# Kernel tuning notes

Measured on AMD Instinct MI355X. Metric: run time of the kernel, lower is better.

Reference implementation:

```python
import jax, jax.numpy as jnp
import numpy as np
jax.config.update("jax_enable_x64", True)  # int64 hash codes for lattice keys

N_KPTS = 32768
C = 61      # feature channels; f-MLP input dim is C+3 = 64
D = 64      # disp-distribution channels
D_LAT = 8   # last f-layer output -> permutohedral position dim

# large odd 62-bit multipliers for the lattice-key hash (wraps mod 2^64)
_MULTS = np.array([2654435761405764093, 1181783497276652981,
                   3202034522624059733, 2685821657736338717,
                   1876998521354586173, 1481765933965188213,
                   2549297995355413921, 3373259426345127233], dtype=np.int64)


def _hcode(k, mults):
    return jnp.sum(k.astype(jnp.int64) * mults, axis=-1)


def _pl_filter(pos, vals):
    """Permutohedral lattice splat -> blur -> slice (approx. Gaussian filter).
    pos: (N, d) float32 lattice positions, vals: (N, vd) float32 values."""
    N, d = pos.shape
    vd = vals.shape[1]
    M = N * (d + 1)  # fixed-size hash table (every point touches d+1 vertices)
    # --- elevate onto hyperplane H_d in R^{d+1} ---
    scale = np.float32(np.sqrt(2.0 / 3.0) * (d + 1)) / np.sqrt(
        np.arange(1, d + 1, dtype=np.float32) * np.arange(2, d + 2, dtype=np.float32))
    E = np.zeros((d + 1, d), dtype=np.float32)
    E[0, :] = 1.0
    for i in range(1, d + 1):
        E[i, i - 1] = -float(i)
        E[i, i:] = 1.0
    elevated = (pos * jnp.asarray(scale, jnp.float32)) @ jnp.asarray(E).T  # (N, d+1)
    # --- nearest zero-colored lattice point and simplex ranks ---
    rem0 = jnp.floor(elevated / (d + 1) + 0.5) * (d + 1)
    sum_val = jnp.round(jnp.sum(rem0, -1) / (d + 1)).astype(jnp.int32)
    diff = elevated - rem0
    rank = jnp.argsort(jnp.argsort(-diff, axis=-1), axis=-1).astype(jnp.int32) + sum_val[:, None]
    lo = rank < 0
    hi = rank > d
    rem0 = rem0 + jnp.where(lo, float(d + 1), 0.0) - jnp.where(hi, float(d + 1), 0.0)
    rank = rank + jnp.where(lo, d + 1, 0) - jnp.where(hi, d + 1, 0)
    # --- barycentric coordinates ---
    t = (elevated - rem0) / (d + 1)
    rows = jnp.arange(N)[:, None]
    bary = jnp.zeros((N, d + 2), jnp.float32)
    bary = bary.at[rows, d - rank].add(t)
    bary = bary.at[rows, d + 1 - rank].add(-t)
    bary = bary.at[:, 0].add(1.0 + bary[:, d + 1])
    w = bary[:, :d + 1]  # (N, d+1) vertex weights
    # --- simplex vertex keys (first d coords; full key sums to 0) ---
    canonical = np.zeros((d + 1, d + 1), np.int32)
    for r in range(d + 1):
        canonical[r, :d + 1 - r] = r
        canonical[r, d + 1 - r:] = r - (d + 1)
    keys = rem0.astype(jnp.int32)[None, :, :d] + jnp.asarray(canonical)[:, rank[:, :d]]  # (d+1,N,d)
    # --- hash table via sorted unique codes (jit-safe fixed size) ---
    mults = jnp.asarray(_MULTS[:d])
    codes = _hcode(keys, mults).reshape(M)
    uniq, inv = jnp.unique(codes, return_inverse=True, size=M,
                           fill_value=jnp.iinfo(jnp.int64).max)
    inv = inv.reshape(M)
    # --- splat ---
    wv = (w.T[:, :, None] * vals[None]).reshape(M, vd)
    lat = jax.ops.segment_sum(wv, inv, num_segments=M)  # (M, vd)
    occ = jax.ops.segment_sum(jnp.ones((M,), jnp.float32), inv, num_segments=M) > 0
    ukeys = jnp.zeros((M, d), jnp.int32).at[inv].set(keys.reshape(M, d))
    # --- blur along each of the d+1 lattice directions ---
    for j in range(d + 1):
        off = np.ones(d + 1, np.int32)
        off[j] = -d
        o = jnp.asarray(off[:d])
        def _nbr(sign, lat=lat):
            c = _hcode(ukeys + sign * o, mults)
            i = jnp.clip(jnp.searchsorted(uniq, c), 0, M - 1)
            ok = (jnp.take(uniq, i) == c) & jnp.take(occ, i)
            return jnp.where(ok[:, None], jnp.take(lat, i, axis=0), 0.0)
        lat = jnp.where(occ[:, None], 0.5 * lat + 0.25 * (_nbr(1) + _nbr(-1)), lat)
    # --- slice ---
    alpha = 1.0 / (1.0 + 2.0 ** (-d))
    return jnp.sum(w.T[:, :, None] * jnp.take(lat, inv, axis=0).reshape(d + 1, N, vd), 0) * alpha


def _layernorm2(x, g, b):
    # LayerNorm(normalized_shape=(N, K)): stats over the last TWO dims jointly
    mu = jnp.mean(x, axis=(-2, -1), keepdims=True)
    var = jnp.mean((x - mu) ** 2, axis=(-2, -1), keepdims=True)
    return (x - mu) * jax.lax.rsqrt(var + 1e-5) * g + b


def setup_inputs() -> dict:
    key = jax.random.key(0)
    ks = jax.random.split(key, 16)
    f32 = jnp.float32
    rn = lambda k, shape, s=1.0: jax.random.normal(k, shape, dtype=f32) * s
    inp = {
        "kpts": rn(ks[0], (1, N_KPTS, 3)),
        "disps_distr": rn(ks[1], (1, N_KPTS, D)),
        "feats": rn(ks[2], (1, N_KPTS, C)),
    }
    i = 3
    for b in range(2):
        inp[f"Wd{b}0"] = rn(ks[i], (D, D), 0.05); i += 1
        inp[f"bd{b}0"] = jnp.zeros((D,), f32)
        inp[f"Wd{b}1"] = rn(ks[i], (D, D), 0.05); i += 1
        inp[f"bd{b}1"] = jnp.zeros((D,), f32)
        inp[f"Wf{b}"] = rn(ks[i], (C + 3, D_LAT), 0.1); i += 1
        inp[f"bf{b}"] = jnp.zeros((D_LAT,), f32)
        inp[f"g{b}"] = jnp.ones((N_KPTS, D_LAT), f32)
        inp[f"be{b}"] = jnp.zeros((N_KPTS, D_LAT), f32)
    return inp


def reference(kpts, disps_distr, feats, Wd00, bd00, Wd01, bd01, Wf0, bf0, g0, be0,
              Wd10, bd10, Wd11, bd11, Wf1, bf1, g1, be1):
    fk = jnp.concatenate([kpts, feats], axis=-1)  # (1, N, C+3)
    x = jnp.reshape(disps_distr, (1, N_KPTS, -1))
    blocks = [(Wd00, bd00, Wd01, bd01, Wf0, bf0, g0, be0),
              (Wd10, bd10, Wd11, bd11, Wf1, bf1, g1, be1)]
    for (Wd0, bd0, Wd1, bd1, Wf, bf, g, be) in blocks:
        x = jax.nn.relu(x @ Wd0 + bd0)   # d-layer 0
        x = jax.nn.relu(x @ Wd1 + bd1)   # d-layer 1
        # only the LAST f-layer output is used by the torch code (feats_kpts is never updated)
        pos = _layernorm2(jax.nn.relu(fk @ Wf + bf), g, be)  # (1, N, 8)
        x = _pl_filter(pos[0], x[0])[None]
    return x
```

## Files before the change

kernel.cpp:

```cpp
#include <hip/hip_runtime.h>
#include <hip/hip_bf16.h>
#include <hip/hip_fp16.h>
#include <stdint.h>

typedef unsigned long long u64;

#define NK 32768
#define DL 8
#define DP1 9
#define MT (NK*DP1)
#define HBITS 19
#define HSIZE (1u<<HBITS)
#define HMASK (HSIZE-1)
#define EMPTY_CODE 0xFFFFFFFFFFFFFFFFULL
#define NBLK 1152
#define HBLK (HSIZE/256)
#define CAP 32
#define MAXHUB 16384

__device__ __constant__ u64 c_mults[8] = {
    2654435761405764093ULL, 1181783497276652981ULL, 3202034522624059733ULL,
    2685821657736338717ULL, 1876998521354586173ULL, 1481765933965188213ULL,
    2549297995355413921ULL, 3373259426345127233ULL};

__device__ __forceinline__ unsigned int hmix(u64 x) {
    return (unsigned int)(x >> (64 - HBITS)) & HMASK;
}

__device__ __forceinline__ u64 dir_delta(int j) {
    u64 s = 0;
    #pragma unroll
    for (int k = 0; k < 8; k++) s += c_mults[k];
    return (j == 8) ? s : (s - 9ULL * c_mults[j]);
}

__device__ __forceinline__ float ldf(const void* p, int i, int bf) {
    if (bf) return __bfloat162float(((const __hip_bfloat16*)p)[i]);
    return ((const float*)p)[i];
}

__global__ void k_detect(const unsigned* __restrict__ g0w, int* __restrict__ flag) {
    if (threadIdx.x == 0) {
        int f = 1;
        for (int i = 0; i < 8; i++) if (g0w[i] != 0x3F803F80u) f = 0;
        *flag = f;
    }
}

__global__ __launch_bounds__(256) void k_mlp(const void* __restrict__ xin, int use_df_in,
    const void* __restrict__ W0, const void* __restrict__ B0,
    const void* __restrict__ W1, const void* __restrict__ B1,
    float* __restrict__ xout, const int* __restrict__ df, double* __restrict__ stats) {
    __shared__ float w0[64*64], w1[64*64], xs[16][64], y1[16][64];
    int bf = *df;
    int bfin = use_df_in ? bf : 0;
    int tid = threadIdx.x;
    int row0 = blockIdx.x * 16;
    if (blockIdx.x == 0 && tid == 0) { stats[0] = 0.0; stats[1] = 0.0; }
    for (int i = tid; i < 4096; i += 256) { w0[i] = ldf(W0, i, bf); w1[i] = ldf(W1, i, bf); }
    for (int i = tid; i < 1024; i += 256) xs[i>>6][i&63] = ldf(xin, row0*64 + i, bfin);
    __syncthreads();
    int rb = tid >> 6, col = tid & 63;
    float b0c = ldf(B0, col, bf);
    float a0 = b0c, a1 = b0c, a2 = b0c, a3 = b0c;
    #pragma unroll
    for (int k = 0; k < 64; k++) {
        float w = w0[k*64+col];
        a0 = fmaf(xs[rb   ][k], w, a0);
        a1 = fmaf(xs[rb+ 4][k], w, a1);
        a2 = fmaf(xs[rb+ 8][k], w, a2);
        a3 = fmaf(xs[rb+12][k], w, a3);
    }
    y1[rb   ][col] = fmaxf(a0, 0.f);
    y1[rb+ 4][col] = fmaxf(a1, 0.f);
    y1[rb+ 8][col] = fmaxf(a2, 0.f);
    y1[rb+12][col] = fmaxf(a3, 0.f);
    __syncthreads();
    float b1c = ldf(B1, col, bf);
    a0 = b1c; a1 = b1c; a2 = b1c; a3 = b1c;
    #pragma unroll
    for (int k = 0; k < 64; k++) {
        float w = w1[k*64+col];
        a0 = fmaf(y1[rb   ][k], w, a0);
        a1 = fmaf(y1[rb+ 4][k], w, a1);
        a2 = fmaf(y1[rb+ 8][k], w, a2);
        a3 = fmaf(y1[rb+12][k], w, a3);
    }
    xout[(row0+rb   )*64 + col] = fmaxf(a0, 0.f);
    xout[(row0+rb+ 4)*64 + col] = fmaxf(a1, 0.f);
    xout[(row0+rb+ 8)*64 + col] = fmaxf(a2, 0.f);
    xout[(row0+rb+12)*64 + col] = fmaxf(a3, 0.f);
}

__global__ __launch_bounds__(256) void k_pos(const void* __restrict__ kpts,
    const void* __restrict__ feats, const void* __restrict__ Wf,
    const void* __restrict__ Bf, float* __restrict__ pos_pre,
    double* __restrict__ stats, const int* __restrict__ df) {
    __shared__ float wf[64*8];
    __shared__ float fk[32][65];
    __shared__ float red[256], red2[256];
    int bf = *df;
    int tid = threadIdx.x;
    int n0 = blockIdx.x * 32;
    for (int i = tid; i < 512; i += 256) wf[i] = ldf(Wf, i, bf);
    for (int i = tid; i < 32*64; i += 256) {
        int pt = i >> 6, k = i & 63, n = n0 + pt;
        fk[pt][k] = (k < 3) ? ldf(kpts, n*3 + k, bf) : ldf(feats, n*61 + (k-3), bf);
    }
    __syncthreads();
    int pt = tid >> 3, j = tid & 7, n = n0 + pt;
    float acc = ldf(Bf, j, bf);
    #pragma unroll
    for (int k = 0; k < 64; k++) acc = fmaf(fk[pt][k], wf[k*8+j], acc);
    acc = fmaxf(acc, 0.f);
    pos_pre[n*8 + j] = acc;
    red[tid] = acc; red2[tid] = acc * acc;
    __syncthreads();
    for (int s = 128; s > 0; s >>= 1) {
        if (tid < s) { red[tid] += red[tid+s]; red2[tid] += red2[tid+s]; }
        __syncthreads();
    }
    if (tid == 0) { atomicAdd(&stats[0], (double)red[0]); atomicAdd(&stats[1], (double)red2[0]); }
}

__global__ __launch_bounds__(256) void k_embed(const float* __restrict__ pos_pre,
    const double* __restrict__ stats, const void* __restrict__ g,
    const void* __restrict__ be, float* __restrict__ wgt,
    u64* __restrict__ pcodes, int* __restrict__ cnt, int* __restrict__ cnt2,
    int* __restrict__ hubid, const int* __restrict__ df) {
    int bf = *df;
    int n = blockIdx.x * 256 + threadIdx.x;
    if (n >= NK) return;
    const double inv_cnt = 1.0 / (double)(NK * DL);
    double mud = stats[0] * inv_cnt;
    double vard = stats[1] * inv_cnt - mud * mud;
    float mu = (float)mud;
    float rs = rsqrtf((float)vard + 1e-5f);
    const float scale[8] = {
        5.196152422706632f, 3.0f, 2.1213203435596424f, 1.643167672515498f,
        1.3416407864998738f, 1.1338934190276817f, 0.9819805060619657f, 0.8660254037844386f};
    float c[8];
    #pragma unroll
    for (int k = 0; k < 8; k++) {
        float v = pos_pre[n*8 + k];
        float p = (v - mu) * rs * ldf(g, n*8 + k, bf) + ldf(be, n*8 + k, bf);
        c[k] = p * scale[k];
    }
    float sufa[9]; sufa[8] = 0.f;
    #pragma unroll
    for (int k = 7; k >= 0; k--) sufa[k] = sufa[k+1] + c[k];
    float elev[9];
    elev[0] = sufa[0];
    #pragma unroll
    for (int i = 1; i < 9; i++) elev[i] = sufa[i] - (float)i * c[i-1];
    int ri[9], sumv = 0;
    float diff[9];
    #pragma unroll
    for (int i = 0; i < 9; i++) {
        ri[i] = (int)floorf(elev[i] / 9.0f + 0.5f);
        sumv += ri[i];
        diff[i] = elev[i] - 9.f * (float)ri[i];
    }
    int rank[9];
    #pragma unroll
    for (int i = 0; i < 9; i++) {
        int r = 0;
        #pragma unroll
        for (int j = 0; j < 9; j++)
            r += (diff[j] > diff[i]) || ((diff[j] == diff[i]) && (j < i));
        rank[i] = r + sumv;
    }
    #pragma unroll
    for (int i = 0; i < 9; i++) {
        if (rank[i] < 0)      { rank[i] += 9; ri[i] += 1; }
        else if (rank[i] > 8) { rank[i] -= 9; ri[i] -= 1; }
    }
    float t[9];
    #pragma unroll
    for (int i = 0; i < 9; i++) t[i] = (elev[i] - 9.f * (float)ri[i]) / 9.f;
    float bary[10];
    #pragma unroll
    for (int i = 0; i < 10; i++) bary[i] = 0.f;
    #pragma unroll
    for (int i = 0; i < 9; i++) { bary[8 - rank[i]] += t[i]; bary[9 - rank[i]] -= t[i]; }
    bary[0] += 1.f + bary[9];
    for (int r = 0; r < 9; r++) {
        u64 code = 0;
        #pragma unroll
        for (int k = 0; k < 8; k++) {
            int key = 9 * ri[k] + ((rank[k] <= 8 - r) ? r : (r - 9));
            code += (u64)(long long)key * c_mults[k];
        }
        int m = n * 9 + r;
        wgt[m] = bary[r];
        pcodes[m] = code;
        cnt[m] = 0;
        cnt2[m] = 0;
        hubid[m] = -1;
    }
}

__global__ __launch_bounds__(256) void k_insert(const u64* __restrict__ pcodes,
    u64* __restrict__ htab_code, unsigned int* __restrict__ ppos) {
    int m = blockIdx.x * 256 + threadIdx.x;
    if (m >= MT) return;
    u64 code = pcodes[m];
    unsigned int pos = hmix(code);
    for (;;) {
        u64 cc = htab_code[pos];
        if (cc == code) break;
        if (cc == EMPTY_CODE) {
            u64 old = atomicCAS(&htab_code[pos], EMPTY_CODE, code);
            if (old == EMPTY_CODE || old == code) break;
        }
        pos = (pos + 1) & HMASK;
    }
    ppos[m] = pos;
}

__global__ __launch_bounds__(256) void k_occ(const u64* __restrict__ htab_code,
    int* __restrict__ bocc) {
    __shared__ int wcnt[4];
    unsigned int i = blockIdx.x * 256 + threadIdx.x;
    bool occ = (htab_code[i] != EMPTY_CODE);
    u64 mask = __ballot(occ);
    int lane = threadIdx.x & 63;
    if (lane == 0) wcnt[threadIdx.x >> 6] = __popcll(mask);
    __syncthreads();
    if (threadIdx.x == 0) bocc[blockIdx.x] = wcnt[0] + wcnt[1] + wcnt[2] + wcnt[3];
}

__global__ __launch_bounds__(256) void k_occscan(int* __restrict__ bocc,
    int* __restrict__ counter, int* __restrict__ nhub) {
    __shared__ int s[256];
    __shared__ int carry;
    int t = threadIdx.x;
    if (t == 0) { carry = 0; *nhub = 0; }
    __syncthreads();
    for (int c = 0; c < HBLK / 256; c++) {
        int i = c * 256 + t;
        int v = bocc[i];
        s[t] = v; __syncthreads();
        for (int off = 1; off < 256; off <<= 1) {
            int a = (t >= off) ? s[t-off] : 0;
            __syncthreads();
            s[t] += a;
            __syncthreads();
        }
        int cl = carry;
        bocc[i] = s[t] - v + cl;
        __syncthreads();
        if (t == 0) carry = cl + s[255];
        __syncthreads();
    }
    if (t == 0) *counter = carry;
}

__global__ __launch_bounds__(256) void k_assign2(const u64* __restrict__ htab_code,
    const int* __restrict__ bocc, int* __restrict__ htab_slot,
    u64* __restrict__ slot_code) {
    __shared__ int wbase[4];
    unsigned int i = blockIdx.x * 256 + threadIdx.x;
    u64 cde = htab_code[i];
    bool occ = (cde != EMPTY_CODE);
    int lane = threadIdx.x & 63;
    int wid  = threadIdx.x >> 6;
    u64 mask = __ballot(occ);
    int prefix = __popcll(mask & ((1ULL << lane) - 1ULL));
    if (lane == 0) wbase[wid] = __popcll(mask);
    __syncthreads();
    if (threadIdx.x == 0) {
        int run = bocc[blockIdx.x];
        for (int w = 0; w < 4; w++) { int c = wbase[w]; wbase[w] = run; run += c; }
    }
    __syncthreads();
    if (occ) {
        int s = wbase[wid] + prefix;
        htab_slot[i] = s;
        slot_code[s] = cde;
    }
}

__global__ __launch_bounds__(256) void k_nbr(const u64* __restrict__ slot_code,
    const u64* __restrict__ htab_code, const int* __restrict__ htab_slot,
    const int* __restrict__ counter, int2* __restrict__ nbr) {
    int idx = blockIdx.x * 256 + threadIdx.x;
    if (idx >= 9 * MT) return;
    int j = idx / MT;
    int sl = idx - j * MT;
    int count = *counter;
    if (sl >= count) return;
    u64 dj = dir_delta(j);
    u64 code = slot_code[sl];
    int res[2];
    #pragma unroll
    for (int s = 0; s < 2; s++) {
        u64 cde = code + (s ? (u64)(0ULL - dj) : dj);
        unsigned int pos = hmix(cde);
        int r = -1;
        for (;;) {
            u64 cc = htab_code[pos];
            if (cc == cde) { r = htab_slot[pos]; break; }
            if (cc == EMPTY_CODE) break;
            pos = (pos + 1) & HMASK;
        }
        res[s] = r;
    }
    nbr[j * MT + sl] = make_int2(res[0], res[1]);
}

__global__ __launch_bounds__(256) void k_lookup(const unsigned int* __restrict__ ppos,
    const int* __restrict__ htab_slot, int* __restrict__ sidx, int* __restrict__ cnt) {
    int m = blockIdx.x * 256 + threadIdx.x;
    if (m >= MT) return;
    int s = htab_slot[ppos[m]];
    sidx[m] = s;
    atomicAdd(&cnt[s], 1);
}

__global__ __launch_bounds__(256) void k_scan1(const int* __restrict__ cnt,
    int* __restrict__ exbuf, int* __restrict__ bsum,
    int* __restrict__ hublist, int* __restrict__ hubid, int* __restrict__ nhub) {
    __shared__ int s[256];
    int t = threadIdx.x;
    int i = blockIdx.x * 256 + t;
    int v = cnt[i];
    if (v > CAP) {
        int h = atomicAdd(nhub, 1);
        if (h < MAXHUB) { hublist[h] = i; hubid[i] = h; }
    }
    s[t] = v; __syncthreads();
    for (int off = 1; off < 256; off <<= 1) {
        int a = (t >= off) ? s[t-off] : 0;
        __syncthreads();
        s[t] += a;
        __syncthreads();
    }
    exbuf[i] = s[t] - v;
    if (t == 255) bsum[blockIdx.x] = s[255];
}

__global__ __launch_bounds__(256) void k_scan2(int* __restrict__ bsum) {
    __shared__ int s[256];
    __shared__ int carry;
    int t = threadIdx.x;
    if (t == 0) carry = 0;
    __syncthreads();
    for (int c = 0; c < (NBLK + 255) / 256; c++) {
        int i = c * 256 + t;
        int v = (i < NBLK) ? bsum[i] : 0;
        s[t] = v; __syncthreads();
        for (int off = 1; off < 256; off <<= 1) {
            int a = (t >= off) ? s[t-off] : 0;
            __syncthreads();
            s[t] += a;
            __syncthreads();
        }
        int cl = carry;
        if (i < NBLK) bsum[i] = s[t] - v + cl;
        __syncthreads();
        if (t == 0) carry = cl + s[255];
        __syncthreads();
    }
}

__global__ __launch_bounds__(256) void k_scatter(const int* __restrict__ sidx,
    const int* __restrict__ exbuf, const int* __restrict__ bsum,
    int* __restrict__ cnt2, int* __restrict__ list) {
    int m = blockIdx.x * 256 + threadIdx.x;
    if (m < MT) {
        int s = sidx[m];
        int ofs = atomicAdd(&cnt2[s], 1);
        list[exbuf[s] + bsum[s >> 8] + ofs] = m;
    }
}

__global__ __launch_bounds__(256) void k_splat_a(const float* __restrict__ xbuf,
    const float* __restrict__ wgt, const int* __restrict__ exbuf,
    const int* __restrict__ bsum, const int* __restrict__ cnt,
    const int* __restrict__ list, __half* __restrict__ val,
    const int* __restrict__ counter) {
    int count = *counter;
    int sl = blockIdx.x * 8 + (threadIdx.x >> 5);
    int lane = threadIdx.x & 31;
    if (sl >= count) return;
    int c = cnt[sl];
    if (c > CAP) return;
    int st = exbuf[sl] + bsum[sl >> 8];
    const float2* x2 = (const float2*)xbuf;
    float2 acc = make_float2(0.f, 0.f);
    int mm = 0; float ww = 0.f;
    if (lane < c) { mm = list[st + lane]; ww = wgt[mm]; }
    for (int k = 0; k < c; k++) {
        int   m = __shfl(mm, k, 32);
        float w = __shfl(ww, k, 32);
        float2 xv = x2[(m / 9) * 32 + lane];
        acc.x = fmaf(w, xv.x, acc.x);
        acc.y = fmaf(w, xv.y, acc.y);
    }
    ((__half2*)val)[(size_t)sl * 32 + lane] = __float22half2_rn(acc);
}

__global__ __launch_bounds__(256) void k_splat_b(const float* __restrict__ xbuf,
    const float* __restrict__ wgt, const int* __restrict__ sidx,
    const int* __restrict__ cnt, const int* __restrict__ list,
    const int* __restrict__ hubid, float* __restrict__ hubval) {
    int chunk = blockIdx.x * 8 + (threadIdx.x >> 5);
    int lane = threadIdx.x & 31;
    int e = chunk * 32 + lane;
    int m = 0, hid = -1; float w = 0.f; int hub = 0;
    if (e < MT) {
        m = list[e];
        int slot = sidx[m];
        hub = (cnt[slot] > CAP);
        if (hub) { w = wgt[m]; hid = hubid[slot]; }
    }
    u64 bal = __ballot(hub);
    unsigned int half = (threadIdx.x & 32) ? (unsigned int)(bal >> 32) : (unsigned int)bal;
    if (!half) return;
    const float2* x2 = (const float2*)xbuf;
    float2 acc = make_float2(0.f, 0.f);
    int cur = -1;
    while (half) {
        int k = __ffs(half) - 1; half &= half - 1;
        int   hk = __shfl(hid, k, 32);
        int   mk = __shfl(m, k, 32);
        float wk = __shfl(w, k, 32);
        float2 xv = x2[(mk / 9) * 32 + lane];
        if (hk != cur) {
            if (cur >= 0) {
                atomicAdd(&hubval[(size_t)cur * 64 + 2*lane    ], acc.x);
                atomicAdd(&hubval[(size_t)cur * 64 + 2*lane + 1], acc.y);
            }
            cur = hk; acc = make_float2(0.f, 0.f);
        }
        acc.x = fmaf(wk, xv.x, acc.x);
        acc.y = fmaf(wk, xv.y, acc.y);
    }
    atomicAdd(&hubval[(size_t)cur * 64 + 2*lane    ], acc.x);
    atomicAdd(&hubval[(size_t)cur * 64 + 2*lane + 1], acc.y);
}

__global__ __launch_bounds__(256) void k_hubcvt(const float* __restrict__ hubval,
    const int* __restrict__ hublist, const int* __restrict__ nhub,
    __half* __restrict__ val) {
    int idx = blockIdx.x * 256 + threadIdx.x;
    int hi = idx >> 5, lane = idx & 31;
    if (hi >= *nhub) return;
    int sl = hublist[hi];
    float2 v = ((const float2*)hubval)[(size_t)hi * 32 + lane];
    ((__half2*)val)[(size_t)sl * 32 + lane] = __float22half2_rn(v);
}

__global__ __launch_bounds__(256) void k_blur(const __half* __restrict__ vin,
    __half* __restrict__ vout, const int2* __restrict__ nbrj,
    const int* __restrict__ counter) {
    int idx = blockIdx.x * 256 + threadIdx.x;
    int sl = idx >> 3, lane = idx & 7;
    int count = *counter;
    if (sl >= count) return;
    int2 nbp = nbrj[sl];
    typedef union { uint4 u; __half2 h[4]; } row16;
    const uint4* vin4 = (const uint4*)vin;
    uint4* vout4 = (uint4*)vout;
    row16 S, A, B, O;
    S.u = vin4[(size_t)sl*8 + lane];
    uint4 z; z.x = 0; z.y = 0; z.z = 0; z.w = 0;
    A.u = (nbp.x >= 0) ? vin4[(size_t)nbp.x*8 + lane] : z;
    B.u = (nbp.y >= 0) ? vin4[(size_t)nbp.y*8 + lane] : z;
    #pragma unroll
    for (int k = 0; k < 4; k++) {
        float2 fs = __half22float2(S.h[k]);
        float2 fa = __half22float2(A.h[k]);
        float2 fb = __half22float2(B.h[k]);
        float2 r;
        r.x = 0.5f * fs.x + 0.25f * (fa.x + fb.x);
        r.y = 0.5f * fs.y + 0.25f * (fa.y + fb.y);
        O.h[k] = __float22half2_rn(r);
    }
    vout4[(size_t)sl*8 + lane] = O.u;
}

__global__ __launch_bounds__(256) void k_slice(const float* __restrict__ wgt,
    const int* __restrict__ sidx, const __half* __restrict__ val,
    float* __restrict__ outf, void* __restrict__ outb, int write_out,
    const int* __restrict__ df) {
    int bf = *df;
    int idx = blockIdx.x * 256 + threadIdx.x;
    if (idx >= NK * 64) return;
    int n = idx >> 6, ch = idx & 63;
    float acc = 0.f;
    #pragma unroll
    for (int r = 0; r < 9; r++) {
        int m = n * 9 + r;
        acc = fmaf(wgt[m], __half2float(val[(size_t)sidx[m]*64 + ch]), acc);
    }
    acc *= 0.9961089494163424f;
    if (write_out) {
        if (bf) ((__hip_bfloat16*)outb)[idx] = __float2bfloat16(acc);
        else    ((float*)outb)[idx] = acc;
    } else {
        outf[idx] = acc;
    }
}

extern "C" void kernel_launch(void* const* d_in, const int* in_sizes, int n_in,
                              void* d_out, int out_size, void* d_ws, size_t ws_size,
                              hipStream_t stream) {
    const void* kpts  = d_in[0];
    const void* disps = d_in[1];
    const void* feats = d_in[2];

    char* p = (char*)d_ws;
    float* xbuf     = (float*)p;  p += (size_t)NK*64*4;
    float* pos_pre  = (float*)p;  p += (size_t)NK*8*4;
    double* stats   = (double*)p; p += 256;
    int*   dflag    = (int*)p;    p += 256;
    float* wgt      = (float*)p;  p += (size_t)MT*4;
    int*   sidx     = (int*)p;    p += (size_t)MT*4;
    u64*   pcodes   = (u64*)p;    p += (size_t)MT*8;
    unsigned int* ppos = (unsigned int*)p; p += (size_t)MT*4;
    u64*   htabc    = (u64*)p;    p += (size_t)HSIZE*8;
    int*   htabs    = (int*)p;    p += (size_t)HSIZE*4;
    u64*   slotc    = (u64*)p;    p += (size_t)MT*8;
    int*   counter  = (int*)p;    p += 256;
    int*   nhub     = (int*)p;    p += 256;
    int*   bocc     = (int*)p;    p += (size_t)HBLK*4;
    int*   cnt      = (int*)p;    p += (size_t)MT*4;
    int*   cnt2     = (int*)p;    p += (size_t)MT*4;
    int*   hubid    = (int*)p;    p += (size_t)MT*4;
    int*   exbuf    = (int*)p;    p += (size_t)MT*4;
    int*   list     = (int*)p;    p += (size_t)MT*4;
    int*   bsum     = (int*)p;    p += 256*32;
    int*   hublist  = (int*)p;    p += (size_t)MAXHUB*4;
    float* hubval   = (float*)p;  p += (size_t)MAXHUB*64*4;
    int2*  nbr      = (int2*)p;   p += (size_t)MT*9*8;
    __half* valA    = (__half*)p; p += (size_t)MT*64*2;
    __half* valB    = (__half*)p; p += (size_t)MT*64*2;

    k_detect<<<1, 64, 0, stream>>>((const unsigned*)d_in[3 + 6], dflag);

    for (int b = 0; b < 2; b++) {
        const void* W0 = d_in[3 + b*8 + 0];
        const void* B0 = d_in[3 + b*8 + 1];
        const void* W1 = d_in[3 + b*8 + 2];
        const void* B1 = d_in[3 + b*8 + 3];
        const void* Wf = d_in[3 + b*8 + 4];
        const void* Bf = d_in[3 + b*8 + 5];
        const void* G  = d_in[3 + b*8 + 6];
        const void* Be = d_in[3 + b*8 + 7];

        k_mlp<<<NK/16, 256, 0, stream>>>(b == 0 ? disps : (const void*)xbuf, b == 0 ? 1 : 0,
                                         W0, B0, W1, B1, xbuf, dflag, stats);

        k_pos<<<NK/32, 256, 0, stream>>>(kpts, feats, Wf, Bf, pos_pre, stats, dflag);

        hipMemsetAsync(htabc, 0xFF, (size_t)HSIZE*8, stream);
        hipMemsetAsync(hubval, 0, (size_t)MAXHUB*64*4, stream);

        k_embed<<<NK/256, 256, 0, stream>>>(pos_pre, stats, G, Be, wgt, pcodes,
                                            cnt, cnt2, hubid, dflag);
        k_insert<<<NBLK, 256, 0, stream>>>(pcodes, htabc, ppos);
        k_occ<<<HBLK, 256, 0, stream>>>(htabc, bocc);
        k_occscan<<<1, 256, 0, stream>>>(bocc, counter, nhub);
        k_assign2<<<HBLK, 256, 0, stream>>>(htabc, bocc, htabs, slotc);
        k_nbr<<<(9*MT + 255)/256, 256, 0, stream>>>(slotc, htabc, htabs, counter, nbr);
        k_lookup<<<NBLK, 256, 0, stream>>>(ppos, htabs, sidx, cnt);

        k_scan1<<<NBLK, 256, 0, stream>>>(cnt, exbuf, bsum, hublist, hubid, nhub);
        k_scan2<<<1, 256, 0, stream>>>(bsum);
        k_scatter<<<NBLK, 256, 0, stream>>>(sidx, exbuf, bsum, cnt2, list);
        k_splat_a<<<(MT + 7)/8, 256, 0, stream>>>(xbuf, wgt, exbuf, bsum, cnt, list,
                                                  valA, counter);
        k_splat_b<<<(MT/32 + 7)/8, 256, 0, stream>>>(xbuf, wgt, sidx, cnt, list, hubid, hubval);
        k_hubcvt<<<(MAXHUB*32)/256, 256, 0, stream>>>(hubval, hublist, nhub, valA);

        for (int j = 0; j < 9; j++) {
            const __half* vin = (j & 1) ? valB : valA;
            __half*       vout = (j & 1) ? valA : valB;
            k_blur<<<(MT*8 + 255)/256, 256, 0, stream>>>(vin, vout, nbr + (size_t)j*MT, counter);
        }
        k_slice<<<(NK*64)/256, 256, 0, stream>>>(wgt, sidx, valB, xbuf,
                                                 d_out, b == 1 ? 1 : 0, dflag);
    }
}
```

Before: 774.6 us.

## Merge independent kernels and run blur chain in persistent grid-barrier kernel

Independent kernels (MLP+pos, embed+memsets, nbr+lookup, splat_a+splat_b) are merged into single launches that branch on block index. The hub conversion, the nine blur passes and the slice are fused into one persistent kernel with a software grid barrier, cutting per-block launch overhead and gaps. The persistent kernel uses 1024 blocks and relies on all of them being co-resident; without a cooperative launch this could deadlock if occupancy is lower than assumed. Stats reset moves into the coop kernel for the next block iteration.

```diff
diff --git a/kernel.cpp b/kernel.cpp
--- a/kernel.cpp
+++ b/kernel.cpp
@@ -18,6 +18,16 @@
 #define CAP 32
 #define MAXHUB 16384
 
+#define MLPB (NK/16)
+#define POSB (NK/32)
+#define EMBB (NK/256)
+#define HZB  384
+#define VZB  128
+#define NBRB (9*MT/256)
+#define SPAB (MT/8)
+#define SPBB 1152
+#define COOPB 1024
+
 __device__ __constant__ u64 c_mults[8] = {
     2654435761405764093ULL, 1181783497276652981ULL, 3202034522624059733ULL,
     2685821657736338717ULL, 1876998521354586173ULL, 1481765933965188213ULL,
@@ -39,97 +49,132 @@
     return ((const float*)p)[i];
 }
 
-__global__ void k_detect(const unsigned* __restrict__ g0w, int* __restrict__ flag) {
+__device__ __forceinline__ void gbar(int* bar, int* s_gen) {
+    __syncthreads();
+    if (threadIdx.x == 0) {
+        int g = *s_gen;
+        int nb = (int)gridDim.x;
+        __builtin_amdgcn_fence(__ATOMIC_RELEASE, "agent");
+        int v = __hip_atomic_fetch_add(&bar[0], 1, __ATOMIC_ACQ_REL, __HIP_MEMORY_SCOPE_AGENT);
+        if (v == nb - 1) {
+            __hip_atomic_fetch_add(&bar[0], -nb, __ATOMIC_RELAXED, __HIP_MEMORY_SCOPE_AGENT);
+            __hip_atomic_store(&bar[1], g + 1, __ATOMIC_RELEASE, __HIP_MEMORY_SCOPE_AGENT);
+        } else {
+            while (__hip_atomic_load(&bar[1], __ATOMIC_RELAXED, __HIP_MEMORY_SCOPE_AGENT) == g) {
+                __builtin_amdgcn_s_sleep(8);
+            }
+        }
+        __builtin_amdgcn_fence(__ATOMIC_ACQUIRE, "agent");
+        *s_gen = g + 1;
+    }
+    __syncthreads();
+}
+
+__global__ void k_detect(const unsigned* __restrict__ g0w, int* __restrict__ flag,
+                         double* __restrict__ stats, int* __restrict__ bar) {
     if (threadIdx.x == 0) {
         int f = 1;
         for (int i = 0; i < 8; i++) if (g0w[i] != 0x3F803F80u) f = 0;
         *flag = f;
-    }
-}
-
-__global__ __launch_bounds__(256) void k_mlp(const void* __restrict__ xin, int use_df_in,
+        stats[0] = 0.0; stats[1] = 0.0;
+        bar[0] = 0; bar[1] = 0;
+    }
+}
+
+__global__ __launch_bounds__(256) void k_mlppos(const void* __restrict__ xin, int use_df_in,
     const void* __restrict__ W0, const void* __restrict__ B0,
     const void* __restrict__ W1, const void* __restrict__ B1,
-    float* __restrict__ xout, const int* __restrict__ df, double* __restrict__ stats) {
-    __shared__ float w0[64*64], w1[64*64], xs[16][64], y1[16][64];
-    int bf = *df;
-    int bfin = use_df_in ? bf : 0;
-    int tid = threadIdx.x;
-    int row0 = blockIdx.x * 16;
-    if (blockIdx.x == 0 && tid == 0) { stats[0] = 0.0; stats[1] = 0.0; }
-    for (int i = tid; i < 4096; i += 256) { w0[i] = ldf(W0, i, bf); w1[i] = ldf(W1, i, bf); }
-    for (int i = tid; i < 1024; i += 256) xs[i>>6][i&63] = ldf(xin, row0*64 + i, bfin);
-    __syncthreads();
-    int rb = tid >> 6, col = tid & 63;
-    float b0c = ldf(B0, col, bf);
-    float a0 = b0c, a1 = b0c, a2 = b0c, a3 = b0c;
-    #pragma unroll
-    for (int k = 0; k < 64; k++) {
-        float w = w0[k*64+col];
-        a0 = fmaf(xs[rb   ][k], w, a0);
-        a1 = fmaf(xs[rb+ 4][k], w, a1);
-        a2 = fmaf(xs[rb+ 8][k], w, a2);
-        a3 = fmaf(xs[rb+12][k], w, a3);
-    }
-    y1[rb   ][col] = fmaxf(a0, 0.f);
-    y1[rb+ 4][col] = fmaxf(a1, 0.f);
-    y1[rb+ 8][col] = fmaxf(a2, 0.f);
-    y1[rb+12][col] = fmaxf(a3, 0.f);
-    __syncthreads();
-    float b1c = ldf(B1, col, bf);
-    a0 = b1c; a1 = b1c; a2 = b1c; a3 = b1c;
-    #pragma unroll
-    for (int k = 0; k < 64; k++) {
-        float w = w1[k*64+col];
-        a0 = fmaf(y1[rb   ][k], w, a0);
-        a1 = fmaf(y1[rb+ 4][k], w, a1);
-        a2 = fmaf(y1[rb+ 8][k], w, a2);
-        a3 = fmaf(y1[rb+12][k], w, a3);
-    }
-    xout[(row0+rb   )*64 + col] = fmaxf(a0, 0.f);
-    xout[(row0+rb+ 4)*64 + col] = fmaxf(a1, 0.f);
-    xout[(row0+rb+ 8)*64 + col] = fmaxf(a2, 0.f);
-    xout[(row0+rb+12)*64 + col] = fmaxf(a3, 0.f);
-}
-
-__global__ __launch_bounds__(256) void k_pos(const void* __restrict__ kpts,
-    const void* __restrict__ feats, const void* __restrict__ Wf,
-    const void* __restrict__ Bf, float* __restrict__ pos_pre,
-    double* __restrict__ stats, const int* __restrict__ df) {
-    __shared__ float wf[64*8];
-    __shared__ float fk[32][65];
-    __shared__ float red[256], red2[256];
+    float* __restrict__ xout, const int* __restrict__ df,
+    const void* __restrict__ kpts, const void* __restrict__ feats,
+    const void* __restrict__ Wf, const void* __restrict__ Bf,
+    float* __restrict__ pos_pre, double* __restrict__ stats) {
+    __shared__ union {
+        struct { float w0[4096], w1[4096], xs[16][64], y1[16][64]; } m;
+        struct { float wf[512]; float fk[32][65]; float red[256], red2[256]; } p;
+    } sm;
     int bf = *df;
     int tid = threadIdx.x;
-    int n0 = blockIdx.x * 32;
-    for (int i = tid; i < 512; i += 256) wf[i] = ldf(Wf, i, bf);
-    for (int i = tid; i < 32*64; i += 256) {
-        int pt = i >> 6, k = i & 63, n = n0 + pt;
-        fk[pt][k] = (k < 3) ? ldf(kpts, n*3 + k, bf) : ldf(feats, n*61 + (k-3), bf);
-    }
-    __syncthreads();
-    int pt = tid >> 3, j = tid & 7, n = n0 + pt;
-    float acc = ldf(Bf, j, bf);
-    #pragma unroll
-    for (int k = 0; k < 64; k++) acc = fmaf(fk[pt][k], wf[k*8+j], acc);
-    acc = fmaxf(acc, 0.f);
-    pos_pre[n*8 + j] = acc;
-    red[tid] = acc; red2[tid] = acc * acc;
-    __syncthreads();
-    for (int s = 128; s > 0; s >>= 1) {
-        if (tid < s) { red[tid] += red[tid+s]; red2[tid] += red2[tid+s]; }
-        __syncthreads();
-    }
-    if (tid == 0) { atomicAdd(&stats[0], (double)red[0]); atomicAdd(&stats[1], (double)red2[0]); }
-}
-
-__global__ __launch_bounds__(256) void k_embed(const float* __restrict__ pos_pre,
+    if (blockIdx.x < MLPB) {
+        int bfin = use_df_in ? bf : 0;
+        int row0 = blockIdx.x * 16;
+        for (int i = tid; i < 4096; i += 256) { sm.m.w0[i] = ldf(W0, i, bf); sm.m.w1[i] = ldf(W1, i, bf); }
+        for (int i = tid; i < 1024; i += 256) sm.m.xs[i>>6][i&63] = ldf(xin, row0*64 + i, bfin);
+        __syncthreads();
+        int rb = tid >> 6, col = tid & 63;
+        float b0c = ldf(B0, col, bf);
+        float a0 = b0c, a1 = b0c, a2 = b0c, a3 = b0c;
+        #pragma unroll
+        for (int k = 0; k < 64; k++) {
+            float w = sm.m.w0[k*64+col];
+            a0 = fmaf(sm.m.xs[rb   ][k], w, a0);
+            a1 = fmaf(sm.m.xs[rb+ 4][k], w, a1);
+            a2 = fmaf(sm.m.xs[rb+ 8][k], w, a2);
+            a3 = fmaf(sm.m.xs[rb+12][k], w, a3);
+        }
+        sm.m.y1[rb   ][col] = fmaxf(a0, 0.f);
+        sm.m.y1[rb+ 4][col] = fmaxf(a1, 0.f);
+        sm.m.y1[rb+ 8][col] = fmaxf(a2, 0.f);
+        sm.m.y1[rb+12][col] = fmaxf(a3, 0.f);
+        __syncthreads();
+        float b1c = ldf(B1, col, bf);
+        a0 = b1c; a1 = b1c; a2 = b1c; a3 = b1c;
+        #pragma unroll
+        for (int k = 0; k < 64; k++) {
+            float w = sm.m.w1[k*64+col];
+            a0 = fmaf(sm.m.y1[rb   ][k], w, a0);
+            a1 = fmaf(sm.m.y1[rb+ 4][k], w, a1);
+            a2 = fmaf(sm.m.y1[rb+ 8][k], w, a2);
+            a3 = fmaf(sm.m.y1[rb+12][k], w, a3);
+        }
+        xout[(row0+rb   )*64 + col] = fmaxf(a0, 0.f);
+        xout[(row0+rb+ 4)*64 + col] = fmaxf(a1, 0.f);
+        xout[(row0+rb+ 8)*64 + col] = fmaxf(a2, 0.f);
+        xout[(row0+rb+12)*64 + col] = fmaxf(a3, 0.f);
+    } else {
+        int n0 = (blockIdx.x - MLPB) * 32;
+        for (int i = tid; i < 512; i += 256) sm.p.wf[i] = ldf(Wf, i, bf);
+        for (int i = tid; i < 32*64; i += 256) {
+            int pt = i >> 6, k = i & 63, n = n0 + pt;
+            sm.p.fk[pt][k] = (k < 3) ? ldf(kpts, n*3 + k, bf) : ldf(feats, n*61 + (k-3), bf);
+        }
+        __syncthreads();
+        int pt = tid >> 3, j = tid & 7, n = n0 + pt;
+        float acc = ldf(Bf, j, bf);
+        #pragma unroll
+        for (int k = 0; k < 64; k++) acc = fmaf(sm.p.fk[pt][k], sm.p.wf[k*8+j], acc);
+        acc = fmaxf(acc, 0.f);
+        pos_pre[n*8 + j] = acc;
+        sm.p.red[tid] = acc; sm.p.red2[tid] = acc * acc;
+        __syncthreads();
+        for (int s = 128; s > 0; s >>= 1) {
+            if (tid < s) { sm.p.red[tid] += sm.p.red[tid+s]; sm.p.red2[tid] += sm.p.red2[tid+s]; }
+            __syncthreads();
+        }
+        if (tid == 0) { atomicAdd(&stats[0], (double)sm.p.red[0]); atomicAdd(&stats[1], (double)sm.p.red2[0]); }
+    }
+}
+
+__global__ __launch_bounds__(256) void k_embedz(const float* __restrict__ pos_pre,
     const double* __restrict__ stats, const void* __restrict__ g,
     const void* __restrict__ be, float* __restrict__ wgt,
     u64* __restrict__ pcodes, int* __restrict__ cnt, int* __restrict__ cnt2,
-    int* __restrict__ hubid, const int* __restrict__ df) {
+    int* __restrict__ hubid, const int* __restrict__ df,
+    u64* __restrict__ htabc, float* __restrict__ hubval) {
+    int bid = blockIdx.x;
+    if (bid >= EMBB) {
+        if (bid < EMBB + HZB) {
+            uint4 f; f.x = 0xFFFFFFFFu; f.y = 0xFFFFFFFFu; f.z = 0xFFFFFFFFu; f.w = 0xFFFFFFFFu;
+            for (int i = (bid - EMBB) * 256 + threadIdx.x; i < (int)(HSIZE/2); i += HZB * 256)
+                ((uint4*)htabc)[i] = f;
+        } else {
+            uint4 z; z.x = 0; z.y = 0; z.z = 0; z.w = 0;
+            for (int i = (bid - EMBB - HZB) * 256 + threadIdx.x; i < MAXHUB*16; i += VZB * 256)
+                ((uint4*)hubval)[i] = z;
+        }
+        return;
+    }
     int bf = *df;
-    int n = blockIdx.x * 256 + threadIdx.x;
+    int n = bid * 256 + threadIdx.x;
     if (n >= NK) return;
     const double inv_cnt = 1.0 / (double)(NK * DL);
     double mud = stats[0] * inv_cnt;
@@ -281,41 +326,41 @@
     }
 }
 
-__global__ __launch_bounds__(256) void k_nbr(const u64* __restrict__ slot_code,
+__global__ __launch_bounds__(256) void k_nbrlookup(const u64* __restrict__ slot_code,
     const u64* __restrict__ htab_code, const int* __restrict__ htab_slot,
-    const int* __restrict__ counter, int2* __restrict__ nbr) {
-    int idx = blockIdx.x * 256 + threadIdx.x;
-    if (idx >= 9 * MT) return;
-    int j = idx / MT;
-    int sl = idx - j * MT;
-    int count = *counter;
-    if (sl >= count) return;
-    u64 dj = dir_delta(j);
-    u64 code = slot_code[sl];
-    int res[2];
-    #pragma unroll
-    for (int s = 0; s < 2; s++) {
-        u64 cde = code + (s ? (u64)(0ULL - dj) : dj);
-        unsigned int pos = hmix(cde);
-        int r = -1;
-        for (;;) {
-            u64 cc = htab_code[pos];
-            if (cc == cde) { r = htab_slot[pos]; break; }
-            if (cc == EMPTY_CODE) break;
-            pos = (pos + 1) & HMASK;
-        }
-        res[s] = r;
-    }
-    nbr[j * MT + sl] = make_int2(res[0], res[1]);
-}
-
-__global__ __launch_bounds__(256) void k_lookup(const unsigned int* __restrict__ ppos,
-    const int* __restrict__ htab_slot, int* __restrict__ sidx, int* __restrict__ cnt) {
-    int m = blockIdx.x * 256 + threadIdx.x;
-    if (m >= MT) return;
-    int s = htab_slot[ppos[m]];
-    sidx[m] = s;
-    atomicAdd(&cnt[s], 1);
+    const int* __restrict__ counter, int2* __restrict__ nbr,
+    const unsigned int* __restrict__ ppos, int* __restrict__ sidx,
+    int* __restrict__ cnt) {
+    if (blockIdx.x < NBRB) {
+        int idx = blockIdx.x * 256 + threadIdx.x;
+        int j = idx / MT;
+        int sl = idx - j * MT;
+        int count = *counter;
+        if (sl >= count) return;
+        u64 dj = dir_delta(j);
+        u64 code = slot_code[sl];
+        int res[2];
+        #pragma unroll
+        for (int s = 0; s < 2; s++) {
+            u64 cde = code + (s ? (u64)(0ULL - dj) : dj);
+            unsigned int pos = hmix(cde);
+            int r = -1;
+            for (;;) {
+                u64 cc = htab_code[pos];
+                if (cc == cde) { r = htab_slot[pos]; break; }
+                if (cc == EMPTY_CODE) break;
+                pos = (pos + 1) & HMASK;
+            }
+            res[s] = r;
+        }
+        nbr[j * MT + sl] = make_int2(res[0], res[1]);
+    } else {
+        int m = (blockIdx.x - NBRB) * 256 + threadIdx.x;
+        if (m >= MT) return;
+        int s = htab_slot[ppos[m]];
+        sidx[m] = s;
+        atomicAdd(&cnt[s], 1);
+    }
 }
 
 __global__ __launch_bounds__(256) void k_scan1(const int* __restrict__ cnt,
@@ -375,132 +420,154 @@
     }
 }
 
-__global__ __launch_bounds__(256) void k_splat_a(const float* __restrict__ xbuf,
+__global__ __launch_bounds__(256) void k_splat(const float* __restrict__ xbuf,
     const float* __restrict__ wgt, const int* __restrict__ exbuf,
     const int* __restrict__ bsum, const int* __restrict__ cnt,
     const int* __restrict__ list, __half* __restrict__ val,
-    const int* __restrict__ counter) {
+    const int* __restrict__ counter, const int* __restrict__ sidx,
+    const int* __restrict__ hubid, float* __restrict__ hubval) {
+    const float2* x2 = (const float2*)xbuf;
+    int lane = threadIdx.x & 31;
+    if (blockIdx.x < SPAB) {
+        int count = *counter;
+        int sl = blockIdx.x * 8 + (threadIdx.x >> 5);
+        if (sl >= count) return;
+        int c = cnt[sl];
+        if (c > CAP) return;
+        int st = exbuf[sl] + bsum[sl >> 8];
+        float2 acc = make_float2(0.f, 0.f);
+        int mm = 0; float ww = 0.f;
+        if (lane < c) { mm = list[st + lane]; ww = wgt[mm]; }
+        for (int k = 0; k < c; k++) {
+            int   m = __shfl(mm, k, 32);
+            float w = __shfl(ww, k, 32);
+            float2 xv = x2[(m / 9) * 32 + lane];
+            acc.x = fmaf(w, xv.x, acc.x);
+            acc.y = fmaf(w, xv.y, acc.y);
+        }
+        ((__half2*)val)[(size_t)sl * 32 + lane] = __float22half2_rn(acc);
+    } else {
+        int chunk = (blockIdx.x - SPAB) * 8 + (threadIdx.x >> 5);
+        int e = chunk * 32 + lane;
+        int m = 0, hid = -1; float w = 0.f; int hub = 0;
+        if (e < MT) {
+            m = list[e];
+            int slot = sidx[m];
+            hub = (cnt[slot] > CAP);
+            if (hub) { w = wgt[m]; hid = hubid[slot]; }
+        }
+        u64 bal = __ballot(hub);
+        unsigned int half = (threadIdx.x & 32) ? (unsigned int)(bal >> 32) : (unsigned int)bal;
+        if (!half) return;
+        float2 acc = make_float2(0.f, 0.f);
+        int cur = -1;
+        while (half) {
+            int k = __ffs(half) - 1; half &= half - 1;
+            int   hk = __shfl(hid, k, 32);
+            int   mk = __shfl(m, k, 32);
+            float wk = __shfl(w, k, 32);
+            float2 xv = x2[(mk / 9) * 32 + lane];
+            if (hk != cur) {
+                if (cur >= 0) {
+                    atomicAdd(&hubval[(size_t)cur * 64 + 2*lane    ], acc.x);
+                    atomicAdd(&hubval[(size_t)cur * 64 + 2*lane + 1], acc.y);
+                }
+                cur = hk; acc = make_float2(0.f, 0.f);
+            }
+            acc.x = fmaf(wk, xv.x, acc.x);
+            acc.y = fmaf(wk, xv.y, acc.y);
+        }
+        atomicAdd(&hubval[(size_t)cur * 64 + 2*lane    ], acc.x);
+        atomicAdd(&hubval[(size_t)cur * 64 + 2*lane + 1], acc.y);
+    }
+}
+
+__global__ __launch_bounds__(256, 4) void k_coop(const float* __restrict__ hubval,
+    const int* __restrict__ hublist, const int* __restrict__ nhub,
+    __half* __restrict__ valA, __half* __restrict__ valB,
+    const int2* __restrict__ nbr, const int* __restrict__ counter,
+    const float* __restrict__ wgt, const int* __restrict__ sidx,
+    float* __restrict__ outf, void* __restrict__ outb, int write_out,
+    const int* __restrict__ df, double* __restrict__ stats,
+    int* __restrict__ bar) {
+    __shared__ int s_gen;
+    if (threadIdx.x == 0)
+        s_gen = __hip_atomic_load(&bar[1], __ATOMIC_RELAXED, __HIP_MEMORY_SCOPE_AGENT);
+    __syncthreads();
+
+    int gsz = (int)gridDim.x * 256;
+    int gtid = (int)blockIdx.x * 256 + threadIdx.x;
+
+    int nh = *nhub;
+    for (int idx = gtid; idx < nh * 32; idx += gsz) {
+        int hi = idx >> 5, lane = idx & 31;
+        int sl = hublist[hi];
+        float2 v = ((const float2*)hubval)[(size_t)hi * 32 + lane];
+        ((__half2*)valA)[(size_t)sl * 32 + lane] = __float22half2_rn(v);
+    }
+    gbar(bar, &s_gen);
+
     int count = *counter;
-    int sl = blockIdx.x * 8 + (threadIdx.x >> 5);
-    int lane = threadIdx.x & 31;
-    if (sl >= count) return;
-    int c = cnt[sl];
-    if (c > CAP) return;
-    int st = exbuf[sl] + bsum[sl >> 8];
-    const float2* x2 = (const float2*)xbuf;
-    float2 acc = make_float2(0.f, 0.f);
-    int mm = 0; float ww = 0.f;
-    if (lane < c) { mm = list[st + lane]; ww = wgt[mm]; }
-    for (int k = 0; k < c; k++) {
-        int   m = __shfl(mm, k, 32);
-        float w = __shfl(ww, k, 32);
-        float2 xv = x2[(m / 9) * 32 + lane];
-        acc.x = fmaf(w, xv.x, acc.x);
-        acc.y = fmaf(w, xv.y, acc.y);
-    }
-    ((__half2*)val)[(size_t)sl * 32 + lane] = __float22half2_rn(acc);
-}
-
-__global__ __launch_bounds__(256) void k_splat_b(const float* __restrict__ xbuf,
-    const float* __restrict__ wgt, const int* __restrict__ sidx,
-    const int* __restrict__ cnt, const int* __restrict__ list,
-    const int* __restrict__ hubid, float* __restrict__ hubval) {
-    int chunk = blockIdx.x * 8 + (threadIdx.x >> 5);
-    int lane = threadIdx.x & 31;
-    int e = chunk * 32 + lane;
-    int m = 0, hid = -1; float w = 0.f; int hub = 0;
-    if (e < MT) {
-        m = list[e];
-        int slot = sidx[m];
-        hub = (cnt[slot] > CAP);
-        if (hub) { w = wgt[m]; hid = hubid[slot]; }
-    }
-    u64 bal = __ballot(hub);
-    unsigned int half = (threadIdx.x & 32) ? (unsigned int)(bal >> 32) : (unsigned int)bal;
-    if (!half) return;
-    const float2* x2 = (const float2*)xbuf;
-    float2 acc = make_float2(0.f, 0.f);
-    int cur = -1;
-    while (half) {
-        int k = __ffs(half) - 1; half &= half - 1;
-        int   hk = __shfl(hid, k, 32);
-        int   mk = __shfl(m, k, 32);
-        float wk = __shfl(w, k, 32);
-        float2 xv = x2[(mk / 9) * 32 + lane];
-        if (hk != cur) {
-            if (cur >= 0) {
-                atomicAdd(&hubval[(size_t)cur * 64 + 2*lane    ], acc.x);
-                atomicAdd(&hubval[(size_t)cur * 64 + 2*lane + 1], acc.y);
+    int items = count * 8;
+    for (int j = 0; j < 9; j++) {
+        const __half* vin = (j & 1) ? valB : valA;
+        __half*       vout = (j & 1) ? valA : valB;
+        const int2* nbrj = nbr + (size_t)j * MT;
+        const uint4* vin4 = (const uint4*)vin;
+        uint4* vout4 = (uint4*)vout;
+        for (int idx = gtid; idx < items; idx += gsz) {
+            int sl = idx >> 3, lane = idx & 7;
+            int2 nbp = nbrj[sl];
+            typedef union { uint4 u; __half2 h[4]; } row16;
+            row16 S, A, B, O;
+            S.u = vin4[(size_t)sl*8 + lane];
+            uint4 z; z.x = 0; z.y = 0; z.z = 0; z.w = 0;
+            A.u = (nbp.x >= 0) ? vin4[(size_t)nbp.x*8 + lane] : z;
+            B.u = (nbp.y >= 0) ? vin4[(size_t)nbp.y*8 + lane] : z;
+            #pragma unroll
+            for (int k = 0; k < 4; k++) {
+                float2 fs = __half22float2(S.h[k]);
+                float2 fa = __half22float2(A.h[k]);
+                float2 fb = __half22float2(B.h[k]);
+                float2 r;
+                r.x = 0.5f * fs.x + 0.25f * (fa.x + fb.x);
+                r.y = 0.5f * fs.y + 0.25f * (fa.y + fb.y);
+                O.h[k] = __float22half2_rn(r);
             }
-            cur = hk; acc = make_float2(0.f, 0.f);
-        }
-        acc.x = fmaf(wk, xv.x, acc.x);
-        acc.y = fmaf(wk, xv.y, acc.y);
-    }
-    atomicAdd(&hubval[(size_t)cur * 64 + 2*lane    ], acc.x);
-    atomicAdd(&hubval[(size_t)cur * 64 + 2*lane + 1], acc.y);
-}
-
-__global__ __launch_bounds__(256) void k_hubcvt(const float* __restrict__ hubval,
-    const int* __restrict__ hublist, const int* __restrict__ nhub,
-    __half* __restrict__ val) {
-    int idx = blockIdx.x * 256 + threadIdx.x;
-    int hi = idx >> 5, lane = idx & 31;
-    if (hi >= *nhub) return;
-    int sl = hublist[hi];
-    float2 v = ((const float2*)hubval)[(size_t)hi * 32 + lane];
-    ((__half2*)val)[(size_t)sl * 32 + lane] = __float22half2_rn(v);
-}
-
-__global__ __launch_bounds__(256) void k_blur(const __half* __restrict__ vin,
-    __half* __restrict__ vout, const int2* __restrict__ nbrj,
-    const int* __restrict__ counter) {
-    int idx = blockIdx.x * 256 + threadIdx.x;
-    int sl = idx >> 3, lane = idx & 7;
-    int count = *counter;
-    if (sl >= count) return;
-    int2 nbp = nbrj[sl];
-    typedef union { uint4 u; __half2 h[4]; } row16;
-    const uint4* vin4 = (const uint4*)vin;
-    uint4* vout4 = (uint4*)vout;
-    row16 S, A, B, O;
-    S.u = vin4[(size_t)sl*8 + lane];
-    uint4 z; z.x = 0; z.y = 0; z.z = 0; z.w = 0;
-    A.u = (nbp.x >= 0) ? vin4[(size_t)nbp.x*8 + lane] : z;
-    B.u = (nbp.y >= 0) ? vin4[(size_t)nbp.y*8 + lane] : z;
-    #pragma unroll
-    for (int k = 0; k < 4; k++) {
-        float2 fs = __half22float2(S.h[k]);
-        float2 fa = __half22float2(A.h[k]);
-        float2 fb = __half22float2(B.h[k]);
-        float2 r;
-        r.x = 0.5f * fs.x + 0.25f * (fa.x + fb.x);
-        r.y = 0.5f * fs.y + 0.25f * (fa.y + fb.y);
-        O.h[k] = __float22half2_rn(r);
-    }
-    vout4[(size_t)sl*8 + lane] = O.u;
-}
-
-__global__ __launch_bounds__(256) void k_slice(const float* __restrict__ wgt,
-    const int* __restrict__ sidx, const __half* __restrict__ val,
-    float* __restrict__ outf, void* __restrict__ outb, int write_out,
-    const int* __restrict__ df) {
+            vout4[(size_t)sl*8 + lane] = O.u;
+        }
+        gbar(bar, &s_gen);
+    }
+
+    if (gtid == 0) { stats[0] = 0.0; stats[1] = 0.0; }
     int bf = *df;
-    int idx = blockIdx.x * 256 + threadIdx.x;
-    if (idx >= NK * 64) return;
-    int n = idx >> 6, ch = idx & 63;
-    float acc = 0.f;
-    #pragma unroll
-    for (int r = 0; r < 9; r++) {
-        int m = n * 9 + r;
-        acc = fmaf(wgt[m], __half2float(val[(size_t)sidx[m]*64 + ch]), acc);
-    }
-    acc *= 0.9961089494163424f;
-    if (write_out) {
-        if (bf) ((__hip_bfloat16*)outb)[idx] = __float2bfloat16(acc);
-        else    ((float*)outb)[idx] = acc;
-    } else {
-        outf[idx] = acc;
+    const __half2* v2 = (const __half2*)valB;
+    for (int idx = gtid; idx < NK * 32; idx += gsz) {
+        int n = idx >> 5, cp = idx & 31;
+        float2 acc = make_float2(0.f, 0.f);
+        #pragma unroll
+        for (int r = 0; r < 9; r++) {
+            int m = n * 9 + r;
+            float w = wgt[m];
+            float2 hv = __half22float2(v2[(size_t)sidx[m]*32 + cp]);
+            acc.x = fmaf(w, hv.x, acc.x);
+            acc.y = fmaf(w, hv.y, acc.y);
+        }
+        acc.x *= 0.9961089494163424f;
+        acc.y *= 0.9961089494163424f;
+        int o = n*64 + cp*2;
+        if (write_out) {
+            if (bf) {
+                __hip_bfloat16* ob = (__hip_bfloat16*)outb;
+                ob[o]   = __float2bfloat16(acc.x);
+                ob[o+1] = __float2bfloat16(acc.y);
+            } else {
+                float* of = (float*)outb;
+                of[o] = acc.x; of[o+1] = acc.y;
+            }
+        } else {
+            outf[o] = acc.x; outf[o+1] = acc.y;
+        }
     }
 }
 
@@ -538,7 +605,9 @@
     __half* valA    = (__half*)p; p += (size_t)MT*64*2;
     __half* valB    = (__half*)p; p += (size_t)MT*64*2;
 
-    k_detect<<<1, 64, 0, stream>>>((const unsigned*)d_in[3 + 6], dflag);
+    int* bar = ((int*)nhub) + 16;
+
+    k_detect<<<1, 64, 0, stream>>>((const unsigned*)d_in[3 + 6], dflag, stats, bar);
 
     for (int b = 0; b < 2; b++) {
         const void* W0 = d_in[3 + b*8 + 0];
@@ -550,37 +619,29 @@
         const void* G  = d_in[3 + b*8 + 6];
         const void* Be = d_in[3 + b*8 + 7];
 
-        k_mlp<<<NK/16, 256, 0, stream>>>(b == 0 ? disps : (const void*)xbuf, b == 0 ? 1 : 0,
-                                         W0, B0, W1, B1, xbuf, dflag, stats);
-
-        k_pos<<<NK/32, 256, 0, stream>>>(kpts, feats, Wf, Bf, pos_pre, stats, dflag);
-
-        hipMemsetAsync(htabc, 0xFF, (size_t)HSIZE*8, stream);
-        hipMemsetAsync(hubval, 0, (size_t)MAXHUB*64*4, stream);
-
-        k_embed<<<NK/256, 256, 0, stream>>>(pos_pre, stats, G, Be, wgt, pcodes,
-                                            cnt, cnt2, hubid, dflag);
+        k_mlppos<<<MLPB + POSB, 256, 0, stream>>>(
+            b == 0 ? disps : (const void*)xbuf, b == 0 ? 1 : 0,
+            W0, B0, W1, B1, xbuf, dflag,
+            kpts, feats, Wf, Bf, pos_pre, stats);
+
+        k_embedz<<<EMBB + HZB + VZB, 256, 0, stream>>>(pos_pre, stats, G, Be, wgt,
+                                                       pcodes, cnt, cnt2, hubid, dflag,
+                                                       htabc, hubval);
         k_insert<<<NBLK, 256, 0, stream>>>(pcodes, htabc, ppos);
         k_occ<<<HBLK, 256, 0, stream>>>(htabc, bocc);
         k_occscan<<<1, 256, 0, stream>>>(bocc, counter, nhub);
         k_assign2<<<HBLK, 256, 0, stream>>>(htabc, bocc, htabs, slotc);
-        k_nbr<<<(9*MT + 255)/256, 256, 0, stream>>>(slotc, htabc, htabs, counter, nbr);
-        k_lookup<<<NBLK, 256, 0, stream>>>(ppos, htabs, sidx, cnt);
+        k_nbrlookup<<<NBRB + NBLK, 256, 0, stream>>>(slotc, htabc, htabs, counter, nbr,
+                                                     ppos, sidx, cnt);
 
         k_scan1<<<NBLK, 256, 0, stream>>>(cnt, exbuf, bsum, hublist, hubid, nhub);
         k_scan2<<<1, 256, 0, stream>>>(bsum);
         k_scatter<<<NBLK, 256, 0, stream>>>(sidx, exbuf, bsum, cnt2, list);
-        k_splat_a<<<(MT + 7)/8, 256, 0, stream>>>(xbuf, wgt, exbuf, bsum, cnt, list,
-                                                  valA, counter);
-        k_splat_b<<<(MT/32 + 7)/8, 256, 0, stream>>>(xbuf, wgt, sidx, cnt, list, hubid, hubval);
-        k_hubcvt<<<(MAXHUB*32)/256, 256, 0, stream>>>(hubval, hublist, nhub, valA);
-
-        for (int j = 0; j < 9; j++) {
-            const __half* vin = (j & 1) ? valB : valA;
-            __half*       vout = (j & 1) ? valA : valB;
-            k_blur<<<(MT*8 + 255)/256, 256, 0, stream>>>(vin, vout, nbr + (size_t)j*MT, counter);
-        }
-        k_slice<<<(NK*64)/256, 256, 0, stream>>>(wgt, sidx, valB, xbuf,
-                                                 d_out, b == 1 ? 1 : 0, dflag);
-    }
-}
+        k_splat<<<SPAB + SPBB, 256, 0, stream>>>(xbuf, wgt, exbuf, bsum, cnt, list,
+                                                 valA, counter, sidx, hubid, hubval);
+
+        k_coop<<<COOPB, 256, 0, stream>>>(hubval, hublist, nhub, valA, valB,
+                                          nbr, counter, wgt, sidx, xbuf,
+                                          d_out, b == 1 ? 1 : 0, dflag, stats, bar);
+    }
+}
```

Measured after the change: 2.387 ms. 208% more time.
